# Kernel optimization log

Hardware: AMD Instinct MI355X
Metric: run time of the kernel (lower is better)

The kernel has to match this reference:

```python
import jax, jax.numpy as jnp
import numpy as np
import math

EPS = 1e-6
P_MIN = 1e-3
P_MAX = 10.0
NUM_ITERS = 3
REG = 1.0
K = 64       # num_clusters
D = 128      # cluster_dim
TOKEN = 256  # token_dim
B, N, C = 8, 8192, 512


def _l2norm(t):
    return t / jnp.clip(jnp.linalg.norm(t, axis=-1, keepdims=True), 1e-12)


def _mlp(h, W1, b1, W2, b2):
    # torch Linear: y = h @ W.T + b ; dropout is identity at eval
    return jax.nn.relu(h @ W1.T + b1) @ W2.T + b2


def _log_otp_solver(log_a, log_b, M, num_iters, reg):
    M = M / reg
    u = jnp.zeros_like(log_a)
    v = jnp.zeros_like(log_b)
    for _ in range(num_iters):  # fixed small iteration count
        u = log_a - jax.scipy.special.logsumexp(M + v[:, None, :], axis=2)
        v = log_b - jax.scipy.special.logsumexp(M + u[:, :, None], axis=1)
    return M + u[:, :, None] + v[:, None, :]


def _get_matching_probs(S, dustbin_score, num_iters, reg):
    b, m, n = S.shape
    dust_row = jnp.broadcast_to(dustbin_score, (b, 1, n)).astype(S.dtype)
    S_aug = jnp.concatenate([S, dust_row], axis=1)  # [b, m+1, n]
    norm = -math.log(n + m)
    log_a = jnp.full((m + 1,), norm, dtype=S.dtype).at[-1].add(math.log(n - m))
    log_a = jnp.broadcast_to(log_a, (b, m + 1))
    log_b = jnp.full((b, n), norm, dtype=S.dtype)
    log_P = _log_otp_solver(log_a, log_b, S_aug, num_iters, reg)
    return log_P - norm


def setup_inputs() -> dict:
    key = jax.random.key(0)
    ks = jax.random.split(key, 8)
    x = jax.random.normal(ks[0], (B, N, C), dtype=jnp.float32)

    def lin(k, fin, fout):
        k1, k2 = jax.random.split(k)
        W = 0.02 * jax.random.normal(k1, (fout, fin), dtype=jnp.float32)
        b = 0.02 * jax.random.normal(k2, (fout,), dtype=jnp.float32)
        return W, b

    tW1, tb1 = lin(ks[1], C, 512)
    tW2, tb2 = lin(ks[2], 512, TOKEN)
    cW1, cb1 = lin(ks[3], C, 512)
    cW2, cb2 = lin(ks[4], 512, D)
    sW1, sb1 = lin(ks[5], C, 512)
    sW2, sb2 = lin(ks[6], 512, K)
    # GeM p param init so that softplus(w)+p_min == 3.0
    gem_w = jnp.array([math.log(math.exp(3.0 - P_MIN) - 1.0)], dtype=jnp.float32)
    dust_bin = jnp.array(1.0, dtype=jnp.float32)
    return dict(x=x, gem_w=gem_w, dust_bin=dust_bin,
                tW1=tW1, tb1=tb1, tW2=tW2, tb2=tb2,
                cW1=cW1, cb1=cb1, cW2=cW2, cb2=cb2,
                sW1=sW1, sb1=sb1, sW2=sW2, sb2=sb2)


def reference(x, gem_w, dust_bin,
              tW1, tb1, tW2, tb2,
              cW1, cb1, cW2, cb2,
              sW1, sb1, sW2, sb2):
    # --- GeM pooling: [B, N, C] -> [B, C] ---
    p = jnp.minimum(jax.nn.softplus(gem_w) + P_MIN, P_MAX)  # [1]
    g = jnp.mean(jnp.clip(x.astype(jnp.float32), EPS, None) ** p, axis=1) ** (1.0 / p)
    g = jnp.where(jnp.isfinite(g), g, jnp.zeros_like(g))

    global_token = _mlp(g, tW1, tb1, tW2, tb2)          # [B, TOKEN]
    local = _mlp(x, cW1, cb1, cW2, cb2)                 # [B, N, D]
    scores = _mlp(x, sW1, sb1, sW2, sb2)                # [B, N, K]

    S = scores.transpose(0, 2, 1)                       # [B, K, N]
    log_P = _get_matching_probs(S, dust_bin, NUM_ITERS, REG)  # [B, K+1, N]
    p_mat = jnp.exp(log_P)[:, :-1, :]                   # drop dustbin -> [B, K, N]

    # aggregated[b, d, k] = sum_n local[b, n, d] * p[b, k, n]  (no O(B*D*K*N) blowup)
    agg = jnp.einsum('bnd,bkn->bdk', local, p_mat).reshape(x.shape[0], -1)  # [B, D*K]

    result = jnp.concatenate([_l2norm(global_token), _l2norm(agg)], axis=-1)
    return _l2norm(result)
```

## Files before the change

kernel.cpp:

```cpp
#include <hip/hip_runtime.h>
#include <hip/hip_bf16.h>
#include <math.h>

#define BB   8
#define NN   8192
#define CC   512
#define DD   128
#define KK   64
#define TOK  256
#define MM   (BB*NN)

typedef unsigned short u16;
typedef __attribute__((ext_vector_type(8))) short short8;
typedef __attribute__((ext_vector_type(4))) float floatx4;

struct PtrSz { const void* p[15]; int sz[15]; };

__device__ __forceinline__ float bf2f(u16 v) {
    union { unsigned u; float f; } x; x.u = ((unsigned)v) << 16; return x.f;
}
__device__ __forceinline__ u16 f2bf(float f) {
    union { float f; unsigned u; } x; x.f = f;
    unsigned r = x.u + 0x7fffu + ((x.u >> 16) & 1u);
    return (u16)(r >> 16);
}
__device__ __forceinline__ float nat_exp2(float a) {
    float r; asm("v_exp_f32 %0, %1" : "=v"(r) : "v"(a)); return r;
}
__device__ __forceinline__ float nat_log2(float a) {
    float r; asm("v_log_f32 %0, %1" : "=v"(r) : "v"(a)); return r;
}
__device__ __forceinline__ void gload16(const void* g, void* l) {
    __builtin_amdgcn_global_load_lds(
        (const __attribute__((address_space(1))) void*)g,
        (__attribute__((address_space(3))) void*)l, 16, 0, 0);
}

__global__ __launch_bounds__(256)
void fill_sentinel(float* __restrict__ out, int n, float val) {
    int i = blockIdx.x*256 + threadIdx.x;
    if (i < n) out[i] = val;
}

__global__ __launch_bounds__(256)
void detect_all(PtrSz ps, int* __restrict__ flags) {
    int i = blockIdx.x;
    const u16* q = (const u16*)ps.p[i];
    int m = ps.sz[i] < 4096 ? ps.sz[i] : 4096;
    __shared__ int cnt;
    if (threadIdx.x == 0) cnt = 0;
    __syncthreads();
    int c = 0;
    for (int j = threadIdx.x; j < m; j += 256) {
        int e = (q[j] >> 7) & 0xFF;
        if (e < 90 || e > 165) c++;
    }
    atomicAdd(&cnt, c);
    __syncthreads();
    if (threadIdx.x == 0) flags[i] = (cnt * 8 > m) ? 1 : 0;
}

#define W_TW1 0
#define W_TB1 262144
#define W_TW2 262656
#define W_TB2 393728
#define W_CW1 393984
#define W_CB1 656128
#define W_CW2 656640
#define W_CB2 722176
#define W_SW1 722304
#define W_SB1 984448
#define W_SW2 984960
#define W_SB2 1017728
#define W_TOTAL 1017792

__global__ __launch_bounds__(256)
void conv_weights(PtrSz ps, const int* __restrict__ flags,
                  u16* __restrict__ wbuf, float* __restrict__ wscal) {
    long gid = (long)blockIdx.x*256 + threadIdx.x;
    if (gid == 0) {
        float vb = bf2f(((const u16*)ps.p[1])[0]);
        float vf = ((const float*)ps.p[1])[0];
        wscal[0] = (fabsf(vb - 2.94694f) < 0.2f) ? vb : vf;
    } else if (gid == 1) {
        float vb = bf2f(((const u16*)ps.p[2])[0]);
        float vf = ((const float*)ps.p[2])[0];
        wscal[1] = (fabsf(vb - 1.0f) < 0.2f) ? vb : vf;
    }
    if (gid >= W_TOTAL) return;
    int idx; long off;
    if      (gid < W_TB1) { idx = 3;  off = W_TW1; }
    else if (gid < W_TW2) { idx = 4;  off = W_TB1; }
    else if (gid < W_TB2) { idx = 5;  off = W_TW2; }
    else if (gid < W_CW1) { idx = 6;  off = W_TB2; }
    else if (gid < W_CB1) { idx = 7;  off = W_CW1; }
    else if (gid < W_CW2) { idx = 8;  off = W_CB1; }
    else if (gid < W_CB2) { idx = 9;  off = W_CW2; }
    else if (gid < W_SW1) { idx = 10; off = W_CB2; }
    else if (gid < W_SB1) { idx = 11; off = W_SW1; }
    else if (gid < W_SW2) { idx = 12; off = W_SB1; }
    else if (gid < W_SB2) { idx = 13; off = W_SW2; }
    else                  { idx = 14; off = W_SB2; }
    long k = gid - off;
    bool f32in = flags[idx] != 0;
    wbuf[gid] = f32in ? f2bf(((const float*)ps.p[idx])[k]) : ((const u16*)ps.p[idx])[k];
}

__global__ __launch_bounds__(256)
void gem_partial(const void* __restrict__ x, const float* __restrict__ wscal,
                 const int* __restrict__ flags, float* __restrict__ gacc) {
    __shared__ float red[4][512];
    int b = blockIdx.x, ny = blockIdx.y;
    int tid  = threadIdx.x;
    int wave = tid >> 6, lane = tid & 63;
    bool f32in = (flags[0] != 0);
    float gw = wscal[0];
    float p  = fminf(log1pf(expf(gw)) + 1e-3f, 10.0f);
    int c0 = lane*8;
    float s[8];
#pragma unroll
    for (int j = 0; j < 8; ++j) s[j] = 0.f;
    size_t base = ((size_t)b*NN + (size_t)ny*64 + wave)*CC + c0;
    if (f32in) {
        const float* xf = (const float*)x;
#pragma unroll 4
        for (int n = 0; n < 64; n += 4) {
            const float* pf = xf + base + (size_t)n*CC;
            float4 x0 = *(const float4*)pf;
            float4 x1 = *(const float4*)(pf + 4);
            float xv[8] = {x0.x,x0.y,x0.z,x0.w,x1.x,x1.y,x1.z,x1.w};
#pragma unroll
            for (int j = 0; j < 8; ++j)
                s[j] += nat_exp2(p * nat_log2(fmaxf(xv[j], 1e-6f)));
        }
    } else {
        const u16* xu = (const u16*)x;
#pragma unroll 4
        for (int n = 0; n < 64; n += 4) {
            short8 v8 = *(const short8*)(xu + base + (size_t)n*CC);
#pragma unroll
            for (int j = 0; j < 8; ++j)
                s[j] += nat_exp2(p * nat_log2(fmaxf(bf2f((u16)v8[j]), 1e-6f)));
        }
    }
#pragma unroll
    for (int j = 0; j < 8; ++j) red[wave][c0 + j] = s[j];
    __syncthreads();
#pragma unroll
    for (int t = 0; t < 2; ++t) {
        int c = tid + t*256;
        float v = red[0][c] + red[1][c] + red[2][c] + red[3][c];
        atomicAdd(&gacc[b*CC + c], v);
    }
}

__global__ __launch_bounds__(512)
void token_mlp(const float* __restrict__ gacc, const u16* __restrict__ wbuf,
               const float* __restrict__ wscal, float* __restrict__ t) {
    __shared__ float gs[CC];
    __shared__ float hs[512];
    int b = blockIdx.x, j = threadIdx.x;
    {
        float gw = wscal[0];
        float p  = fminf(log1pf(expf(gw)) + 1e-3f, 10.0f);
        float m  = gacc[b*CC + j] / (float)NN;
        float r  = powf(m, 1.0f/p);
        if (!isfinite(r)) r = 0.f;
        gs[j] = r;
    }
    __syncthreads();
    {
        float a = bf2f(wbuf[W_TB1 + j]);
        const u16* w = wbuf + W_TW1 + (size_t)j*CC;
        for (int c = 0; c < CC; c += 8) {
            short8 wv = *(const short8*)(w + c);
#pragma unroll
            for (int q = 0; q < 8; ++q) a += gs[c+q]*bf2f((u16)wv[q]);
        }
        hs[j] = fmaxf(a, 0.f);
    }
    __syncthreads();
    if (j < TOK) {
        float a2 = bf2f(wbuf[W_TB2 + j]);
        const u16* w2 = wbuf + W_TW2 + (size_t)j*512;
        for (int c = 0; c < 512; c += 8) {
            short8 wv = *(const short8*)(w2 + c);
#pragma unroll
            for (int q = 0; q < 8; ++q) a2 += hs[c+q]*bf2f((u16)wv[q]);
        }
        t[b*TOK + j] = a2;
    }
}

template<int BN, int MODE, bool RELU, bool ARAW>
__global__ __launch_bounds__(256)
void gemm_bt(const void* __restrict__ A, const u16* __restrict__ W,
             const u16* __restrict__ bias, void* __restrict__ Cout,
             const int* __restrict__ flags, int N, int Ksz, int lda,
             size_t a_base, int bidx_ovr,
             const u16* __restrict__ W_alt, const u16* __restrict__ bias_alt,
             int nsplit) {
    constexpr int WSUB_N = BN/32;
    extern __shared__ char smem[];
    u16* a_lds = (u16*)smem;
    u16* b_lds = (u16*)smem + 128*32;
    const int tid  = threadIdx.x;
    const int wave = tid >> 6, lane = tid & 63;
    const int wm = wave >> 1, wn = wave & 1;

    int bx = blockIdx.x, by = blockIdx.y;
    {
        int nbx = gridDim.x, nby = gridDim.y;
        int nwg = nbx*nby;
        if ((nwg & 7) == 0) {
            int lid = bx + by*nbx;
            int q = nwg >> 3;
            int t = (lid & 7)*q + (lid >> 3);
            by = t % nby;
            bx = t / nby;
        }
    }
    const u16* Wp = W; const u16* bp = bias;
    int byw = by;
    if (W_alt != nullptr && by >= nsplit) { Wp = W_alt; bp = bias_alt; byw = by - nsplit; }
    const int bm0 = bx * 128;
    const int bn0 = by * BN;
    const int bw0 = byw * BN;
    const int fr = lane & 15;
    const int fk = (lane >> 4) * 8;
    const bool f32in = ARAW && (flags[0] != 0);

    floatx4 acc[4][WSUB_N];
#pragma unroll
    for (int i = 0; i < 4; ++i)
#pragma unroll
        for (int j = 0; j < WSUB_N; ++j) acc[i][j] = (floatx4){0.f,0.f,0.f,0.f};

    for (int k0 = 0; k0 < Ksz; k0 += 32) {
        if (f32in) {
#pragma unroll
            for (int part = 0; part < 2; ++part) {
                int chunk = part*256 + tid;
                int row = chunk >> 2, kc = (chunk & 3)*8;
                size_t gidx = a_base + (size_t)(bm0 + row)*lda + k0 + kc;
                const float* pf = (const float*)A + gidx;
                float4 x0 = *(const float4*)pf;
                float4 x1 = *(const float4*)(pf + 4);
                short8 vA;
                vA[0]=(short)f2bf(x0.x); vA[1]=(short)f2bf(x0.y);
                vA[2]=(short)f2bf(x0.z); vA[3]=(short)f2bf(x0.w);
                vA[4]=(short)f2bf(x1.x); vA[5]=(short)f2bf(x1.y);
                vA[6]=(short)f2bf(x1.z); vA[7]=(short)f2bf(x1.w);
                *(short8*)(a_lds + row*32 + kc) = vA;
            }
        } else {
#pragma unroll
            for (int part = 0; part < 2; ++part) {
                int cb = part*256 + wave*64;
                int mych = cb + lane;
                int row = mych >> 2, kc = (mych & 3)*8;
                gload16((const u16*)A + a_base + (size_t)(bm0 + row)*lda + k0 + kc,
                        a_lds + (size_t)cb*8);
            }
        }
#pragma unroll
        for (int part = 0; part < BN/64; ++part) {
            int cb = part*256 + wave*64;
            int mych = cb + lane;
            int row = mych >> 2, kc = (mych & 3)*8;
            gload16(Wp + (size_t)(bw0 + row)*Ksz + k0 + kc,
                    b_lds + (size_t)cb*8);
        }
        __syncthreads();
        short8 af[4], bfr[WSUB_N];
#pragma unroll
        for (int i = 0; i < 4; ++i)
            af[i] = *(const short8*)(a_lds + (wm*64 + i*16 + fr)*32 + fk);
#pragma unroll
        for (int j = 0; j < WSUB_N; ++j)
            bfr[j] = *(const short8*)(b_lds + (wn*WSUB_N*16 + j*16 + fr)*32 + fk);
#pragma unroll
        for (int i = 0; i < 4; ++i)
#pragma unroll
            for (int j = 0; j < WSUB_N; ++j)
                acc[i][j] = __builtin_amdgcn_mfma_f32_16x16x32_bf16(af[i], bfr[j], acc[i][j], 0, 0, 0);
        __syncthreads();
    }

    if constexpr (MODE == 0) {
        u16* C = (u16*)Cout;
#pragma unroll
        for (int i = 0; i < 4; ++i) {
            int row0 = wm*64 + i*16 + ((lane>>4)<<2);
#pragma unroll
            for (int j = 0; j < WSUB_N; ++j) {
                int col = wn*WSUB_N*16 + j*16 + fr;
                float bb = bf2f(bp[bw0+col]);
#pragma unroll
                for (int r = 0; r < 4; ++r) {
                    float v = acc[i][j][r] + bb;
                    if (RELU) v = fmaxf(v, 0.f);
                    C[(size_t)(bm0+row0+r)*N + (bn0+col)] = f2bf(v);
                }
            }
        }
    } else {
        const int bidx = (bidx_ovr >= 0) ? bidx_ovr : (bm0 >> 13);
        const int nin  = bm0 & 8191;
        if constexpr (MODE == 1) {
            u16* tr = (u16*)smem;
#pragma unroll
            for (int i = 0; i < 4; ++i) {
                int row0 = wm*64 + i*16 + ((lane>>4)<<2);
#pragma unroll
                for (int j = 0; j < WSUB_N; ++j) {
                    int col = wn*WSUB_N*16 + j*16 + fr;
                    float bb = bf2f(bp[bw0+col]);
#pragma unroll
                    for (int r = 0; r < 4; ++r) {
                        float v = acc[i][j][r] + bb;
                        if (RELU) v = fmaxf(v, 0.f);
                        tr[col*128 + row0 + r] = f2bf(v);
                    }
                }
            }
            __syncthreads();
            u16* O = (u16*)Cout;
#pragma unroll
            for (int c = 0; c < (BN*128)/256; ++c) {
                int flat = c*256 + tid;
                int dcol = flat >> 7, rr = flat & 127;
                O[(size_t)(bidx*BN + bn0 + dcol)*NN + nin + rr] = tr[dcol*128 + rr];
            }
        } else {
            float* tr = (float*)smem;
#pragma unroll
            for (int i = 0; i < 4; ++i) {
                int row0 = wm*64 + i*16 + ((lane>>4)<<2);
#pragma unroll
                for (int j = 0; j < WSUB_N; ++j) {
                    int col = wn*WSUB_N*16 + j*16 + fr;
                    float bb = bf2f(bp[bw0+col]);
#pragma unroll
                    for (int r = 0; r < 4; ++r) {
                        float v = acc[i][j][r] + bb;
                        if (RELU) v = fmaxf(v, 0.f);
                        tr[col*128 + row0 + r] = v;
                    }
                }
            }
            __syncthreads();
            float* O = (float*)Cout;
#pragma unroll
            for (int c = 0; c < (BN*128)/256; ++c) {
                int flat = c*256 + tid;
                int dcol = flat >> 7, rr = flat & 127;
                O[(size_t)(bidx*BN + bn0 + dcol)*NN + nin + rr] = tr[dcol*128 + rr];
            }
        }
    }
}

__global__ __launch_bounds__(256)
void sink_u(const float* __restrict__ ST, const float* __restrict__ v,
            const float* __restrict__ wscal, float* __restrict__ u) {
    int m = blockIdx.x, b = blockIdx.y, t = threadIdx.x;
    const float norm = -logf(8256.0f);
    float la = (m == 64) ? norm + logf(8128.0f) : norm;
    float dustf = wscal[1];
    const float* vb = v + (size_t)b*NN;
    float r[32];
    float mx = -1e30f;
    if (m < 64) {
        const float* row = ST + ((size_t)b*64 + m)*NN;
#pragma unroll
        for (int i = 0; i < 32; ++i) { int n = t + i*256; r[i] = row[n] + vb[n]; mx = fmaxf(mx, r[i]); }
    } else {
#pragma unroll
        for (int i = 0; i < 32; ++i) { int n = t + i*256; r[i] = dustf + vb[n]; mx = fmaxf(mx, r[i]); }
    }
#pragma unroll
    for (int off = 32; off; off >>= 1) mx = fmaxf(mx, __shfl_xor(mx, off));
    __shared__ float red[4];
    if ((t & 63) == 0) red[t>>6] = mx;
    __syncthreads();
    mx = fmaxf(fmaxf(red[0], red[1]), fmaxf(red[2], red[3]));
    __syncthreads();
    float s = 0.f;
#pragma unroll
    for (int i = 0; i < 32; ++i) s += expf(r[i] - mx);
#pragma unroll
    for (int off = 32; off; off >>= 1) s += __shfl_xor(s, off);
    if ((t & 63) == 0) red[t>>6] = s;
    __syncthreads();
    s = red[0] + red[1] + red[2] + red[3];
    if (t == 0) u[b*65 + m] = la - (mx + logf(s));
}

template<int WP>
__global__ __launch_bounds__(256)
void sink_v_t(const float* __restrict__ ST, const float* __restrict__ u,
              const float* __restrict__ wscal, float* __restrict__ v,
              u16* __restrict__ P) {
    int b = blockIdx.y;
    int n = blockIdx.x*256 + threadIdx.x;
    __shared__ float us[65];
    if (threadIdx.x < 65) us[threadIdx.x] = u[b*65 + threadIdx.x];
    __syncthreads();
    const float norm = -logf(8256.0f);
    float mx = wscal[1] + us[64];
    float s  = 1.0f;
    const float* col = ST + (size_t)b*64*NN + n;
    if (WP) {
        float r[64];
#pragma unroll
        for (int m = 0; m < 64; ++m) {
            r[m] = col[(size_t)m*NN] + us[m];
            float nm = fmaxf(mx, r[m]);
            s = s*expf(mx - nm) + expf(r[m] - nm);
            mx = nm;
        }
        float vn = norm - (mx + logf(s));
        v[(size_t)b*NN + n] = vn;
#pragma unroll
        for (int k = 0; k < 64; ++k)
            P[((size_t)b*64 + k)*NN + n] = f2bf(expf(r[k] + vn - norm));
    } else {
        for (int m = 0; m < 64; ++m) {
            float tv = col[(size_t)m*NN] + us[m];
            float nm = fmaxf(mx, tv);
            s = s*expf(mx - nm) + expf(tv - nm);
            mx = nm;
        }
        v[(size_t)b*NN + n] = norm - (mx + logf(s));
    }
}

__global__ __launch_bounds__(256)
void agg_mfma(const u16* __restrict__ localT, const u16* __restrict__ P,
              float* __restrict__ agg) {
    __shared__ u16 a_lds[128*32];
    __shared__ u16 b_lds[64*32];
    int b = blockIdx.y, ns = blockIdx.x;
    int n0 = ns*256;
    const int tid  = threadIdx.x;
    const int wave = tid >> 6, lane = tid & 63;
    const int wm = wave >> 1, wn = wave & 1;
    const int fr = lane & 15, fk = (lane >> 4)*8;

    floatx4 acc[4][2];
#pragma unroll
    for (int i = 0; i < 4; ++i)
#pragma unroll
        for (int j = 0; j < 2; ++j) acc[i][j] = (floatx4){0.f,0.f,0.f,0.f};

    for (int s = 0; s < 8; ++s) {
        int nk = n0 + s*32;
#pragma unroll
        for (int part = 0; part < 2; ++part) {
            int chunk = part*256 + tid;
            int row = chunk >> 2, kc = (chunk & 3)*8;
            short8 vA = *(const short8*)(localT + ((size_t)b*128 + row)*NN + nk + kc);
            *(short8*)(a_lds + row*32 + kc) = vA;
        }
        {
            int row = tid >> 2, kc = (tid & 3)*8;
            short8 vB = *(const short8*)(P + ((size_t)b*64 + row)*NN + nk + kc);
            *(short8*)(b_lds + row*32 + kc) = vB;
        }
        __syncthreads();
        short8 af[4], bfr[2];
#pragma unroll
        for (int i = 0; i < 4; ++i)
            af[i] = *(const short8*)(a_lds + (wm*64 + i*16 + fr)*32 + fk);
#pragma unroll
        for (int j = 0; j < 2; ++j)
            bfr[j] = *(const short8*)(b_lds + (wn*32 + j*16 + fr)*32 + fk);
#pragma unroll
        for (int i = 0; i < 4; ++i)
#pragma unroll
            for (int j = 0; j < 2; ++j)
                acc[i][j] = __builtin_amdgcn_mfma_f32_16x16x32_bf16(af[i], bfr[j], acc[i][j], 0, 0, 0);
        __syncthreads();
    }
#pragma unroll
    for (int i = 0; i < 4; ++i) {
        int d0 = wm*64 + i*16 + ((lane>>4)<<2);
#pragma unroll
        for (int j = 0; j < 2; ++j) {
            int k = wn*32 + j*16 + fr;
#pragma unroll
            for (int r = 0; r < 4; ++r)
                atomicAdd(&agg[(size_t)b*8192 + (d0+r)*64 + k], acc[i][j][r]);
        }
    }
}

__global__ __launch_bounds__(256)
void finalize_out(const float* __restrict__ tg, const float* __restrict__ agg,
                  float* __restrict__ out) {
    int b = blockIdx.x, tid = threadIdx.x;
    float tv = tg[b*TOK + tid];
    float s1 = tv*tv;
    const float* ab = agg + (size_t)b*8192;
    float av[32];
    float s2 = 0.f;
#pragma unroll
    for (int i = 0; i < 32; ++i) { av[i] = ab[tid + i*256]; s2 += av[i]*av[i]; }
#pragma unroll
    for (int off = 32; off; off >>= 1) { s1 += __shfl_xor(s1, off); s2 += __shfl_xor(s2, off); }
    __shared__ float r1[4], r2[4];
    int wave = tid >> 6, lane = tid & 63;
    if (lane == 0) { r1[wave] = s1; r2[wave] = s2; }
    __syncthreads();
    float S1 = r1[0]+r1[1]+r1[2]+r1[3];
    float S2 = r2[0]+r2[1]+r2[2]+r2[3];
    const float rs2 = 1.41421356237f;
    float sc1 = 1.0f/(fmaxf(sqrtf(S1), 1e-12f)*rs2);
    float sc2 = 1.0f/(fmaxf(sqrtf(S2), 1e-12f)*rs2);
    out[(size_t)b*8448 + tid] = tv*sc1;
#pragma unroll
    for (int i = 0; i < 32; ++i)
        out[(size_t)b*8448 + 256 + tid + i*256] = av[i]*sc2;
}

extern "C" void kernel_launch(void* const* d_in, const int* in_sizes, int n_in,
                              void* d_out, int out_size, void* d_ws, size_t ws_size,
                              hipStream_t stream) {
    float* out = (float*)d_out;

    static const int EXP[15] = {33554432,1,1,262144,512,131072,256,
                                262144,512,65536,128,262144,512,32768,64};
    bool ok = (n_in == 15) && (out_size == 67584);
    if (ok) for (int i = 0; i < 15; ++i) ok = ok && (in_sizes[i] == EXP[i]);
    if (!ok) {
        fill_sentinel<<<264, 256, 0, stream>>>(out, out_size, 0.25f);
        return;
    }
    const size_t NEED_BATCH = 52934656ull;
    if (ws_size < NEED_BATCH) {
        fill_sentinel<<<264, 256, 0, stream>>>(out, out_size, 0.5f);
        return;
    }

    const void* x = d_in[0];
    PtrSz ps;
    for (int i = 0; i < 15; ++i) { ps.p[i] = d_in[i]; ps.sz[i] = in_sizes[i]; }

    char* base = (char*)d_ws;
    float* gacc = (float*)(base + 0);
    float* u    = (float*)(base + 16384);
    float* v    = (float*)(base + 18464);
    float* agg  = (float*)(base + 280608);
    const size_t ZERO_BYTES = 542752;
    float* tglb = (float*)(base + 559136);
    int*   flags= (int*)  (base + 567328);
    float* wscal= (float*)(base + 567392);
    u16*   wbuf = (u16*)  (base + 567424);
    float* ST   = (float*)(base + 2603008);
    u16* localT = (u16*)  (base + 19380224);
    u16* P      = (u16*)  (base + 36157440);
    u16* h1     = (u16*)  (base + 44546048);
    const size_t FULL_NEED  = 44546048ull + 67108864ull;
    const size_t FUSED_NEED = 44546048ull + 134217728ull;
    const bool fused = (ws_size >= FUSED_NEED);
    const bool mono  = (ws_size >= FULL_NEED);

    hipMemsetAsync(d_ws, 0, ZERO_BYTES, stream);

    detect_all<<<15, 256, 0, stream>>>(ps, flags);
    conv_weights<<<3977, 256, 0, stream>>>(ps, flags, wbuf, wscal);

    gem_partial<<<dim3(BB, 128), 256, 0, stream>>>(x, wscal, flags, gacc);
    token_mlp<<<BB, 512, 0, stream>>>(gacc, wbuf, wscal, tglb);

    const int NOSPLIT = 1 << 30;
    if (fused) {
        gemm_bt<128, 0, true,  true ><<<dim3(512, 8), 256, 16384, stream>>>(
            x, wbuf + W_CW1, wbuf + W_CB1, h1, flags, 1024, 512, 512, 0, -1,
            wbuf + W_SW1, wbuf + W_SB1, 4);
        gemm_bt<128, 1, false, false><<<dim3(512, 1), 256, 32768, stream>>>(
            h1, wbuf + W_CW2, wbuf + W_CB2, localT, flags, 128, 512, 1024, 0, -1,
            nullptr, nullptr, NOSPLIT);
        gemm_bt< 64, 2, false, false><<<dim3(512, 1), 256, 32768, stream>>>(
            h1, wbuf + W_SW2, wbuf + W_SB2, ST, flags, 64, 512, 1024, 512, -1,
            nullptr, nullptr, NOSPLIT);
    } else if (mono) {
        gemm_bt<128, 0, true,  true ><<<dim3(512, 4), 256, 16384, stream>>>(
            x, wbuf + W_CW1, wbuf + W_CB1, h1, flags, 512, 512, 512, 0, -1,
            nullptr, nullptr, NOSPLIT);
        gemm_bt<128, 1, false, false><<<dim3(512, 1), 256, 32768, stream>>>(
            h1, wbuf + W_CW2, wbuf + W_CB2, localT, flags, 128, 512, 512, 0, -1,
            nullptr, nullptr, NOSPLIT);
        gemm_bt<128, 0, true,  true ><<<dim3(512, 4), 256, 16384, stream>>>(
            x, wbuf + W_SW1, wbuf + W_SB1, h1, flags, 512, 512, 512, 0, -1,
            nullptr, nullptr, NOSPLIT);
        gemm_bt< 64, 2, false, false><<<dim3(512, 1), 256, 32768, stream>>>(
            h1, wbuf + W_SW2, wbuf + W_SB2, ST, flags, 64, 512, 512, 0, -1,
            nullptr, nullptr, NOSPLIT);
    } else {
        for (int b = 0; b < BB; ++b) {
            size_t ab = (size_t)b*NN*CC;
            gemm_bt<128, 0, true,  true ><<<dim3(64, 4), 256, 16384, stream>>>(
                x, wbuf + W_CW1, wbuf + W_CB1, h1, flags, 512, 512, 512, ab, -1,
                nullptr, nullptr, NOSPLIT);
            gemm_bt<128, 1, false, false><<<dim3(64, 1), 256, 32768, stream>>>(
                h1, wbuf + W_CW2, wbuf + W_CB2, localT, flags, 128, 512, 512, 0, b,
                nullptr, nullptr, NOSPLIT);
            gemm_bt<128, 0, true,  true ><<<dim3(64, 4), 256, 16384, stream>>>(
                x, wbuf + W_SW1, wbuf + W_SB1, h1, flags, 512, 512, 512, ab, -1,
                nullptr, nullptr, NOSPLIT);
            gemm_bt< 64, 2, false, false><<<dim3(64, 1), 256, 32768, stream>>>(
                h1, wbuf + W_SW2, wbuf + W_SB2, ST, flags, 64, 512, 512, 0, b,
                nullptr, nullptr, NOSPLIT);
        }
    }

    for (int it = 0; it < 3; ++it) {
        sink_u<<<dim3(65, BB), 256, 0, stream>>>(ST, v, wscal, u);
        if (it == 2)
            sink_v_t<1><<<dim3(32, BB), 256, 0, stream>>>(ST, u, wscal, v, P);
        else
            sink_v_t<0><<<dim3(32, BB), 256, 0, stream>>>(ST, u, wscal, v, P);
    }

    agg_mfma<<<dim3(32, BB), 256, 0, stream>>>(localT, P, agg);
    finalize_out<<<BB, 256, 0, stream>>>(tglb, agg, out);
}
```

Measured before the change: 507.6 us.

## Widen GEMM k-tile to 64 with XOR-swizzled LDS and fuse Sinkhorn u-update

The bf16 MFMA GEMM now stages 64-wide k slices per iteration, with an XOR swizzle on the LDS layout to avoid bank conflicts. This halves the number of barriers per k loop but doubles LDS use to 32KB for the first-layer GEMMs. The Sinkhorn loop also drops two of the three sink_u passes over ST. Each v-pass instead emits per-wave partial log-sum-exp statistics for the u update, using u_new = u_old + la - lse(M+u_old+v), and a small sink_comb kernel combines them, which saves re-reading the 64xN score matrix.

Result: slower. 640.5 us (+26.2%).

```diff
diff --git a/kernel.cpp b/kernel.cpp
--- a/kernel.cpp
+++ b/kernel.cpp
@@ -201,9 +201,11 @@
              const u16* __restrict__ W_alt, const u16* __restrict__ bias_alt,
              int nsplit) {
     constexpr int WSUB_N = BN/32;
+    constexpr int APARTS = 4;
+    constexpr int BPARTS = BN/32;
     extern __shared__ char smem[];
     u16* a_lds = (u16*)smem;
-    u16* b_lds = (u16*)smem + 128*32;
+    u16* b_lds = (u16*)smem + 128*64;
     const int tid  = threadIdx.x;
     const int wave = tid >> 6, lane = tid & 63;
     const int wm = wave >> 1, wn = wave & 1;
@@ -236,12 +238,12 @@
 #pragma unroll
         for (int j = 0; j < WSUB_N; ++j) acc[i][j] = (floatx4){0.f,0.f,0.f,0.f};
 
-    for (int k0 = 0; k0 < Ksz; k0 += 32) {
+    for (int k0 = 0; k0 < Ksz; k0 += 64) {
         if (f32in) {
 #pragma unroll
-            for (int part = 0; part < 2; ++part) {
-                int chunk = part*256 + tid;
-                int row = chunk >> 2, kc = (chunk & 3)*8;
+            for (int part = 0; part < APARTS; ++part) {
+                int l = part*256 + tid;
+                int row = l >> 3, kc = (l & 7)*8;
                 size_t gidx = a_base + (size_t)(bm0 + row)*lda + k0 + kc;
                 const float* pf = (const float*)A + gidx;
                 float4 x0 = *(const float4*)pf;
@@ -251,39 +253,49 @@
                 vA[2]=(short)f2bf(x0.z); vA[3]=(short)f2bf(x0.w);
                 vA[4]=(short)f2bf(x1.x); vA[5]=(short)f2bf(x1.y);
                 vA[6]=(short)f2bf(x1.z); vA[7]=(short)f2bf(x1.w);
-                *(short8*)(a_lds + row*32 + kc) = vA;
+                int dst = l ^ ((l >> 3) & 7);
+                *(short8*)(a_lds + dst*8) = vA;
             }
         } else {
 #pragma unroll
-            for (int part = 0; part < 2; ++part) {
+            for (int part = 0; part < APARTS; ++part) {
                 int cb = part*256 + wave*64;
-                int mych = cb + lane;
-                int row = mych >> 2, kc = (mych & 3)*8;
+                int tc = cb + lane;
+                int s  = tc ^ ((tc >> 3) & 7);
+                int row = s >> 3, kc = (s & 7)*8;
                 gload16((const u16*)A + a_base + (size_t)(bm0 + row)*lda + k0 + kc,
                         a_lds + (size_t)cb*8);
             }
         }
 #pragma unroll
-        for (int part = 0; part < BN/64; ++part) {
+        for (int part = 0; part < BPARTS; ++part) {
             int cb = part*256 + wave*64;
-            int mych = cb + lane;
-            int row = mych >> 2, kc = (mych & 3)*8;
+            int tc = cb + lane;
+            int s  = tc ^ ((tc >> 3) & 7);
+            int row = s >> 3, kc = (s & 7)*8;
             gload16(Wp + (size_t)(bw0 + row)*Ksz + k0 + kc,
                     b_lds + (size_t)cb*8);
         }
         __syncthreads();
-        short8 af[4], bfr[WSUB_N];
-#pragma unroll
-        for (int i = 0; i < 4; ++i)
-            af[i] = *(const short8*)(a_lds + (wm*64 + i*16 + fr)*32 + fk);
-#pragma unroll
-        for (int j = 0; j < WSUB_N; ++j)
-            bfr[j] = *(const short8*)(b_lds + (wn*WSUB_N*16 + j*16 + fr)*32 + fk);
-#pragma unroll
-        for (int i = 0; i < 4; ++i)
-#pragma unroll
-            for (int j = 0; j < WSUB_N; ++j)
-                acc[i][j] = __builtin_amdgcn_mfma_f32_16x16x32_bf16(af[i], bfr[j], acc[i][j], 0, 0, 0);
+#pragma unroll
+        for (int kk = 0; kk < 2; ++kk) {
+            short8 af[4], bfr[WSUB_N];
+#pragma unroll
+            for (int i = 0; i < 4; ++i) {
+                int row = wm*64 + i*16 + fr;
+                af[i] = *(const short8*)(a_lds + row*64 + ((kk*32 + fk) ^ ((row & 7) << 3)));
+            }
+#pragma unroll
+            for (int j = 0; j < WSUB_N; ++j) {
+                int row = wn*WSUB_N*16 + j*16 + fr;
+                bfr[j] = *(const short8*)(b_lds + row*64 + ((kk*32 + fk) ^ ((row & 7) << 3)));
+            }
+#pragma unroll
+            for (int i = 0; i < 4; ++i)
+#pragma unroll
+                for (int j = 0; j < WSUB_N; ++j)
+                    acc[i][j] = __builtin_amdgcn_mfma_f32_16x16x32_bf16(af[i], bfr[j], acc[i][j], 0, 0, 0);
+        }
         __syncthreads();
     }
 
@@ -397,43 +409,64 @@
     if (t == 0) u[b*65 + m] = la - (mx + logf(s));
 }
 
-template<int WP>
+template<int MODE_V>
 __global__ __launch_bounds__(256)
 void sink_v_t(const float* __restrict__ ST, const float* __restrict__ u,
               const float* __restrict__ wscal, float* __restrict__ v,
-              u16* __restrict__ P) {
+              u16* __restrict__ P, float2* __restrict__ up) {
     int b = blockIdx.y;
     int n = blockIdx.x*256 + threadIdx.x;
     __shared__ float us[65];
     if (threadIdx.x < 65) us[threadIdx.x] = u[b*65 + threadIdx.x];
     __syncthreads();
     const float norm = -logf(8256.0f);
-    float mx = wscal[1] + us[64];
+    float dustf = wscal[1];
+    float mx = dustf + us[64];
     float s  = 1.0f;
     const float* col = ST + (size_t)b*64*NN + n;
-    if (WP) {
-        float r[64];
-#pragma unroll
-        for (int m = 0; m < 64; ++m) {
-            r[m] = col[(size_t)m*NN] + us[m];
-            float nm = fmaxf(mx, r[m]);
-            s = s*expf(mx - nm) + expf(r[m] - nm);
-            mx = nm;
-        }
-        float vn = norm - (mx + logf(s));
+    float r[64];
+#pragma unroll
+    for (int m = 0; m < 64; ++m) {
+        r[m] = col[(size_t)m*NN] + us[m];
+        float nm = fmaxf(mx, r[m]);
+        s = s*expf(mx - nm) + expf(r[m] - nm);
+        mx = nm;
+    }
+    float vn = norm - (mx + logf(s));
+    if (MODE_V == 2) {
         v[(size_t)b*NN + n] = vn;
 #pragma unroll
         for (int k = 0; k < 64; ++k)
             P[((size_t)b*64 + k)*NN + n] = f2bf(expf(r[k] + vn - norm));
     } else {
-        for (int m = 0; m < 64; ++m) {
-            float tv = col[(size_t)m*NN] + us[m];
-            float nm = fmaxf(mx, tv);
-            s = s*expf(mx - nm) + expf(tv - nm);
-            mx = nm;
-        }
-        v[(size_t)b*NN + n] = norm - (mx + logf(s));
-    }
+        int slice = blockIdx.x*4 + (threadIdx.x >> 6);
+        float2* pb = up + (size_t)b*65*128;
+        for (int m = 0; m < 65; ++m) {
+            float w = (m < 64 ? r[m] : dustf) + vn;
+            float wmx = w;
+#pragma unroll
+            for (int off = 32; off; off >>= 1) wmx = fmaxf(wmx, __shfl_xor(wmx, off));
+            float ws = expf(w - wmx);
+#pragma unroll
+            for (int off = 32; off; off >>= 1) ws += __shfl_xor(ws, off);
+            if ((threadIdx.x & 63) == 0) pb[m*128 + slice] = make_float2(wmx, ws);
+        }
+    }
+}
+
+__global__ __launch_bounds__(128)
+void sink_comb(const float2* __restrict__ up, float* __restrict__ u) {
+    int b = blockIdx.x, t = threadIdx.x;
+    if (t >= 65) return;
+    const float2* pp = up + ((size_t)b*65 + t)*128;
+    float gmx = -1e30f;
+    for (int i = 0; i < 128; ++i) gmx = fmaxf(gmx, pp[i].x);
+    float gs = 0.f;
+    for (int i = 0; i < 128; ++i) gs += pp[i].y * expf(pp[i].x - gmx);
+    const float norm = -logf(8256.0f);
+    float la = (t == 64) ? norm + logf(8128.0f) : norm;
+    float uo = (t < 64) ? u[b*65 + t] : 0.f;
+    u[b*65 + t] = la - (gmx + logf(gs)) + uo;
 }
 
 __global__ __launch_bounds__(256)
@@ -561,6 +594,7 @@
     u16* localT = (u16*)  (base + 19380224);
     u16* P      = (u16*)  (base + 36157440);
     u16* h1     = (u16*)  (base + 44546048);
+    float2* up  = (float2*)h1;
     const size_t FULL_NEED  = 44546048ull + 67108864ull;
     const size_t FUSED_NEED = 44546048ull + 134217728ull;
     const bool fused = (ws_size >= FUSED_NEED);
@@ -576,7 +610,7 @@
 
     const int NOSPLIT = 1 << 30;
     if (fused) {
-        gemm_bt<128, 0, true,  true ><<<dim3(512, 8), 256, 16384, stream>>>(
+        gemm_bt<128, 0, true,  true ><<<dim3(512, 8), 256, 32768, stream>>>(
             x, wbuf + W_CW1, wbuf + W_CB1, h1, flags, 1024, 512, 512, 0, -1,
             wbuf + W_SW1, wbuf + W_SB1, 4);
         gemm_bt<128, 1, false, false><<<dim3(512, 1), 256, 32768, stream>>>(
@@ -586,13 +620,13 @@
             h1, wbuf + W_SW2, wbuf + W_SB2, ST, flags, 64, 512, 1024, 512, -1,
             nullptr, nullptr, NOSPLIT);
     } else if (mono) {
-        gemm_bt<128, 0, true,  true ><<<dim3(512, 4), 256, 16384, stream>>>(
+        gemm_bt<128, 0, true,  true ><<<dim3(512, 4), 256, 32768, stream>>>(
             x, wbuf + W_CW1, wbuf + W_CB1, h1, flags, 512, 512, 512, 0, -1,
             nullptr, nullptr, NOSPLIT);
         gemm_bt<128, 1, false, false><<<dim3(512, 1), 256, 32768, stream>>>(
             h1, wbuf + W_CW2, wbuf + W_CB2, localT, flags, 128, 512, 512, 0, -1,
             nullptr, nullptr, NOSPLIT);
-        gemm_bt<128, 0, true,  true ><<<dim3(512, 4), 256, 16384, stream>>>(
+        gemm_bt<128, 0, true,  true ><<<dim3(512, 4), 256, 32768, stream>>>(
             x, wbuf + W_SW1, wbuf + W_SB1, h1, flags, 512, 512, 512, 0, -1,
             nullptr, nullptr, NOSPLIT);
         gemm_bt< 64, 2, false, false><<<dim3(512, 1), 256, 32768, stream>>>(
@@ -601,13 +635,13 @@
     } else {
         for (int b = 0; b < BB; ++b) {
             size_t ab = (size_t)b*NN*CC;
-            gemm_bt<128, 0, true,  true ><<<dim3(64, 4), 256, 16384, stream>>>(
+            gemm_bt<128, 0, true,  true ><<<dim3(64, 4), 256, 32768, stream>>>(
                 x, wbuf + W_CW1, wbuf + W_CB1, h1, flags, 512, 512, 512, ab, -1,
                 nullptr, nullptr, NOSPLIT);
             gemm_bt<128, 1, false, false><<<dim3(64, 1), 256, 32768, stream>>>(
                 h1, wbuf + W_CW2, wbuf + W_CB2, localT, flags, 128, 512, 512, 0, b,
                 nullptr, nullptr, NOSPLIT);
-            gemm_bt<128, 0, true,  true ><<<dim3(64, 4), 256, 16384, stream>>>(
+            gemm_bt<128, 0, true,  true ><<<dim3(64, 4), 256, 32768, stream>>>(
                 x, wbuf + W_SW1, wbuf + W_SB1, h1, flags, 512, 512, 512, ab, -1,
                 nullptr, nullptr, NOSPLIT);
             gemm_bt< 64, 2, false, false><<<dim3(64, 1), 256, 32768, stream>>>(
@@ -616,13 +650,12 @@
         }
     }
 
-    for (int it = 0; it < 3; ++it) {
-        sink_u<<<dim3(65, BB), 256, 0, stream>>>(ST, v, wscal, u);
-        if (it == 2)
-            sink_v_t<1><<<dim3(32, BB), 256, 0, stream>>>(ST, u, wscal, v, P);
-        else
-            sink_v_t<0><<<dim3(32, BB), 256, 0, stream>>>(ST, u, wscal, v, P);
-    }
+    sink_u<<<dim3(65, BB), 256, 0, stream>>>(ST, v, wscal, u);
+    sink_v_t<1><<<dim3(32, BB), 256, 0, stream>>>(ST, u, wscal, v, P, up);
+    sink_comb<<<BB, 128, 0, stream>>>(up, u);
+    sink_v_t<1><<<dim3(32, BB), 256, 0, stream>>>(ST, u, wscal, v, P, up);
+    sink_comb<<<BB, 128, 0, stream>>>(up, u);
+    sink_v_t<2><<<dim3(32, BB), 256, 0, stream>>>(ST, u, wscal, v, P, up);
 
     agg_mfma<<<dim3(32, BB), 256, 0, stream>>>(localT, P, agg);
     finalize_out<<<BB, 256, 0, stream>>>(tglb, agg, out);
```
